# Optimization experiments

Measured on AMD Instinct MI355X. Metric: run time of the kernel, lower is better.

## Reference

```python
import jax, jax.numpy as jnp
import numpy as np

B, T, D, H = 4, 1024, 1024, 16
DH = D // H  # 64

def setup_inputs() -> dict:
    key = jax.random.key(0)
    ks = jax.random.split(key, 5)
    s = 1.0 / np.sqrt(D)
    return {
        "x": jax.random.normal(ks[0], (B, T, D), dtype=jnp.float32),
        "Wqkv": jax.random.uniform(ks[1], (D, 3 * D), dtype=jnp.float32, minval=-s, maxval=s),
        "bqkv": jax.random.uniform(ks[2], (3 * D,), dtype=jnp.float32, minval=-s, maxval=s),
        "Wproj": jax.random.uniform(ks[3], (D, D), dtype=jnp.float32, minval=-s, maxval=s),
        "bproj": jax.random.uniform(ks[4], (D,), dtype=jnp.float32, minval=-s, maxval=s),
        "mask": jnp.ones((B, T), dtype=jnp.int32),
    }

def reference(x, Wqkv, bqkv, Wproj, bproj, mask):
    Bx, Tx, C = x.shape
    qkv = x @ Wqkv + bqkv                      # [B,T,3D]
    q, k, v = jnp.split(qkv, 3, axis=-1)
    # [B,H,T,DH]
    q = q.reshape(Bx, Tx, H, DH).transpose(0, 2, 1, 3)
    k = k.reshape(Bx, Tx, H, DH).transpose(0, 2, 1, 3)
    v = v.reshape(Bx, Tx, H, DH).transpose(0, 2, 1, 3)
    att = jnp.einsum("bhqd,bhkd->bhqk", q, k) / np.sqrt(DH)
    causal = jnp.tril(jnp.ones((Tx, Tx), dtype=bool))          # [T,T]
    keep = causal[None, None] & (mask[:, None, None, :] != 0)  # [B,1,T,T] broadcast
    att = jnp.where(keep, att, -jnp.inf)
    att = jax.nn.softmax(att, axis=-1)
    # dropout is identity in eval / p=0
    out = jnp.einsum("bhqk,bhkd->bhqd", att, v)                # [B,H,T,DH]
    out = out.transpose(0, 2, 1, 3).reshape(Bx, Tx, C)
    return out @ Wproj + bproj
```

## Files before the change

kernel.cpp:

```cpp
#include <hip/hip_runtime.h>
#include <hip/hip_bf16.h>
#include <cstddef>
#include <cstdint>

#define Bb 4
#define Tt 1024
#define Dd 1024
#define Hh 16

typedef __bf16 bf16x8 __attribute__((ext_vector_type(8)));
typedef __bf16 bf16x4 __attribute__((ext_vector_type(4)));
typedef float  f32x4  __attribute__((ext_vector_type(4)));

__device__ __forceinline__ void gload16(const void* g, void* l) {
    __builtin_amdgcn_global_load_lds(
        (const __attribute__((address_space(1))) void*)g,
        (__attribute__((address_space(3))) void*)l, 16, 0, 0);
}

__global__ __launch_bounds__(256) void prep(const float* __restrict__ x,
                                            const float* __restrict__ Wqkv,
                                            const float* __restrict__ Wproj,
                                            __bf16* __restrict__ xb,
                                            __bf16* __restrict__ wqT,
                                            __bf16* __restrict__ wpT) {
    const int bid = blockIdx.x;
    if (bid < 4096) {
        int i = bid * 256 + threadIdx.x;
        float4 v = ((const float4*)x)[i];
        bf16x4 o = { (__bf16)v.x, (__bf16)v.y, (__bf16)v.z, (__bf16)v.w };
        ((bf16x4*)xb)[i] = o;
        return;
    }
    __shared__ float ld[64][65];
    const float* in;
    __bf16* out;
    int K, N, k0, n0;
    if (bid < 4096 + 768) {
        int j = bid - 4096;
        in = Wqkv; out = wqT; K = 1024; N = 3072;
        k0 = (j & 15) * 64; n0 = (j >> 4) * 64;
    } else {
        int j = bid - 4096 - 768;
        in = Wproj; out = wpT; K = 1024; N = 1024;
        k0 = (j & 15) * 64; n0 = (j >> 4) * 64;
    }
    #pragma unroll
    for (int i = 0; i < 16; i++) {
        int idx = i * 256 + threadIdx.x;
        int r = idx >> 6, c = idx & 63;
        ld[r][c] = in[(size_t)(k0 + r) * N + n0 + c];
    }
    __syncthreads();
    #pragma unroll
    for (int i = 0; i < 16; i++) {
        int idx = i * 256 + threadIdx.x;
        int r = idx >> 6, c = idx & 63;
        out[(size_t)(n0 + r) * K + k0 + c] = (__bf16)ld[c][r];
    }
}

__global__ __launch_bounds__(256) void v_transpose(const __bf16* __restrict__ qkv,
                                                   __bf16* __restrict__ vt) {
    __shared__ __bf16 ld[64][65];
    const int t0 = blockIdx.x * 64;
    const int h  = blockIdx.y;
    const int b  = blockIdx.z;
    const size_t src = ((size_t)(b * Tt + t0)) * 3072 + 2048 + h * 64;
    #pragma unroll
    for (int i = 0; i < 16; i++) {
        int idx = i * 256 + threadIdx.x;
        int tr = idx >> 6, dc = idx & 63;
        ld[tr][dc] = qkv[src + (size_t)tr * 3072 + dc];
    }
    __syncthreads();
    const size_t dst = ((size_t)((b * Hh + h) * 64)) * Tt + t0;
    #pragma unroll
    for (int i = 0; i < 16; i++) {
        int idx = i * 256 + threadIdx.x;
        int dr = idx >> 6, tc = idx & 63;
        vt[dst + (size_t)dr * Tt + tc] = ld[tc][dr];
    }
}

__global__ __launch_bounds__(256) void gemm_bf16(const __bf16* __restrict__ A,
                                                 const __bf16* __restrict__ Bt,
                                                 const float* __restrict__ bias,
                                                 void* __restrict__ Cout,
                                                 int M, int N, int K, int mode) {
    __shared__ __align__(16) __bf16 As[128 * 64];
    __shared__ __align__(16) __bf16 Bs[128 * 64];
    const int tid  = threadIdx.x;
    const int lane = tid & 63;
    const int wave = tid >> 6;
    const int wy = wave >> 1, wx = wave & 1;
    const int l15 = lane & 15, quad = lane >> 4;
    const size_t row0 = (size_t)blockIdx.y * 128;
    const size_t col0 = (size_t)blockIdx.x * 128;

    f32x4 acc[4][4] = {};

    for (int k0 = 0; k0 < K; k0 += 64) {
        #pragma unroll
        for (int i = 0; i < 4; i++) {
            int c = i * 256 + tid;
            int r = c >> 3, seg = (c & 7) ^ (r & 7);
            gload16(&A[(row0 + r) * K + k0 + seg * 8], &As[c * 8]);
        }
        #pragma unroll
        for (int i = 0; i < 4; i++) {
            int c = i * 256 + tid;
            int r = c >> 3, seg = (c & 7) ^ (r & 7);
            gload16(&Bt[(col0 + r) * K + k0 + seg * 8], &Bs[c * 8]);
        }
        __syncthreads();
        #pragma unroll
        for (int kc = 0; kc < 2; kc++) {
            bf16x8 af[4], bfr[4];
            #pragma unroll
            for (int i = 0; i < 4; i++)
                af[i] = *(const bf16x8*)&As[(wy * 64 + i * 16 + l15) * 64 +
                                            (((kc * 4 + quad) ^ (l15 & 7)) * 8)];
            #pragma unroll
            for (int j = 0; j < 4; j++)
                bfr[j] = *(const bf16x8*)&Bs[(wx * 64 + j * 16 + l15) * 64 +
                                             (((kc * 4 + quad) ^ (l15 & 7)) * 8)];
            #pragma unroll
            for (int i = 0; i < 4; i++)
                #pragma unroll
                for (int j = 0; j < 4; j++)
                    acc[i][j] = __builtin_amdgcn_mfma_f32_16x16x32_bf16(af[i], bfr[j], acc[i][j], 0, 0, 0);
        }
        __syncthreads();
    }

    #pragma unroll
    for (int j = 0; j < 4; j++) {
        const size_t col = col0 + wx * 64 + j * 16 + l15;
        const float bj = bias[col];
        const float scale = (mode == 1 && col < 1024) ? 0.125f : 1.0f;
        #pragma unroll
        for (int i = 0; i < 4; i++) {
            const size_t row = row0 + wy * 64 + i * 16 + quad * 4;
            #pragma unroll
            for (int r = 0; r < 4; r++) {
                float v = (acc[i][j][r] + bj) * scale;
                if (mode == 1) ((__bf16*)Cout)[(row + r) * N + col] = (__bf16)v;
                else           ((float*)Cout)[(row + r) * N + col] = v;
            }
        }
    }
}

__global__ __launch_bounds__(256) void gemm_bf16_n64(const __bf16* __restrict__ A,
                                                     const __bf16* __restrict__ Bt,
                                                     const float* __restrict__ bias,
                                                     float* __restrict__ Cout,
                                                     int M, int N, int K) {
    __shared__ __align__(16) __bf16 As[128 * 64];
    __shared__ __align__(16) __bf16 Bs[64 * 64];
    const int tid  = threadIdx.x;
    const int lane = tid & 63;
    const int wave = tid >> 6;
    const int wy = wave >> 1, wx = wave & 1;
    const int l15 = lane & 15, quad = lane >> 4;
    const size_t row0 = (size_t)blockIdx.y * 128;
    const size_t col0 = (size_t)blockIdx.x * 64;

    f32x4 acc[4][2] = {};

    for (int k0 = 0; k0 < K; k0 += 64) {
        #pragma unroll
        for (int i = 0; i < 4; i++) {
            int c = i * 256 + tid;
            int r = c >> 3, seg = (c & 7) ^ (r & 7);
            gload16(&A[(row0 + r) * K + k0 + seg * 8], &As[c * 8]);
        }
        #pragma unroll
        for (int i = 0; i < 2; i++) {
            int c = i * 256 + tid;
            int r = c >> 3, seg = (c & 7) ^ (r & 7);
            gload16(&Bt[(col0 + r) * K + k0 + seg * 8], &Bs[c * 8]);
        }
        __syncthreads();
        #pragma unroll
        for (int kc = 0; kc < 2; kc++) {
            bf16x8 af[4], bfr[2];
            #pragma unroll
            for (int i = 0; i < 4; i++)
                af[i] = *(const bf16x8*)&As[(wy * 64 + i * 16 + l15) * 64 +
                                            (((kc * 4 + quad) ^ (l15 & 7)) * 8)];
            #pragma unroll
            for (int j = 0; j < 2; j++)
                bfr[j] = *(const bf16x8*)&Bs[(wx * 32 + j * 16 + l15) * 64 +
                                             (((kc * 4 + quad) ^ (l15 & 7)) * 8)];
            #pragma unroll
            for (int i = 0; i < 4; i++)
                #pragma unroll
                for (int j = 0; j < 2; j++)
                    acc[i][j] = __builtin_amdgcn_mfma_f32_16x16x32_bf16(af[i], bfr[j], acc[i][j], 0, 0, 0);
        }
        __syncthreads();
    }

    #pragma unroll
    for (int j = 0; j < 2; j++) {
        const size_t col = col0 + wx * 32 + j * 16 + l15;
        const float bj = bias[col];
        #pragma unroll
        for (int i = 0; i < 4; i++) {
            const size_t row = row0 + wy * 64 + i * 16 + quad * 4;
            #pragma unroll
            for (int r = 0; r < 4; r++)
                Cout[(row + r) * N + col] = acc[i][j][r] + bj;
        }
    }
}

__global__ __launch_bounds__(256, 4) void attn_mfma(const __bf16* __restrict__ qkv,
                                                    const __bf16* __restrict__ vt,
                                                    const int* __restrict__ mask,
                                                    __bf16* __restrict__ att) {
    __shared__ __align__(16) __bf16 Ks[2][4096];
    __shared__ __align__(16) __bf16 Vs[2][4096];
    __shared__ __align__(16) __bf16 Ps[4][1024];

    const int h  = blockIdx.x & 15;
    const int b  = blockIdx.x >> 4;
    const int qt = 15 - blockIdx.y;
    const int tid = threadIdx.x, lane = tid & 63, wave = tid >> 6;
    const int l15 = lane & 15, quad = lane >> 4;

    #pragma unroll
    for (int i = 0; i < 2; i++) {
        int c = i * 256 + tid;
        int rr = c >> 3, ch = c & 7;
        gload16(&qkv[((size_t)(b * Tt + qt * 64 + rr)) * 3072 + h * 64 + ((ch ^ (rr & 7)) * 8)],
                &Ks[0][c * 8]);
    }
    __syncthreads();
    bf16x8 qf0 = *(const bf16x8*)&Ks[0][(wave * 16 + l15) * 64 + ((quad ^ (l15 & 7)) * 8)];
    bf16x8 qf1 = *(const bf16x8*)&Ks[0][(wave * 16 + l15) * 64 + (((4 + quad) ^ (l15 & 7)) * 8)];
    __syncthreads();

    #pragma unroll
    for (int i = 0; i < 2; i++) {
        int c = i * 256 + tid;
        int rr = c >> 3, ch = c & 7, sw = ((ch ^ (rr & 7)) * 8);
        gload16(&qkv[((size_t)(b * Tt + rr)) * 3072 + 1024 + h * 64 + sw], &Ks[0][c * 8]);
        gload16(&vt[((size_t)((b * Hh + h) * 64 + rr)) * Tt + sw], &Vs[0][c * 8]);
    }

    f32x4 Oacc[4] = {};
    float lsum = 0.0f;

    for (int kt = 0; kt <= qt; kt++) {
        __syncthreads();
        const int cur = kt & 1;
        if (kt < qt) {
            #pragma unroll
            for (int i = 0; i < 2; i++) {
                int c = i * 256 + tid;
                int rr = c >> 3, ch = c & 7, sw = ((ch ^ (rr & 7)) * 8);
                gload16(&qkv[((size_t)(b * Tt + (kt + 1) * 64 + rr)) * 3072 + 1024 + h * 64 + sw],
                        &Ks[cur ^ 1][c * 8]);
                gload16(&vt[((size_t)((b * Hh + h) * 64 + rr)) * Tt + (kt + 1) * 64 + sw],
                        &Vs[cur ^ 1][c * 8]);
            }
        }

        int mv4[4][4];
        #pragma unroll
        for (int j = 0; j < 4; j++) {
            const int4 m4 = *(const int4*)&mask[b * Tt + kt * 64 + j * 16 + quad * 4];
            mv4[j][0] = m4.x; mv4[j][1] = m4.y; mv4[j][2] = m4.z; mv4[j][3] = m4.w;
        }

        bf16x8 ak[4][2];
        #pragma unroll
        for (int j = 0; j < 4; j++)
            #pragma unroll
            for (int kc = 0; kc < 2; kc++)
                ak[j][kc] = *(const bf16x8*)&Ks[cur][(j * 16 + l15) * 64 +
                                                     (((kc * 4 + quad) ^ (l15 & 7)) * 8)];
        #pragma unroll
        for (int j = 0; j < 4; j++) {
            f32x4 st = {};
            st = __builtin_amdgcn_mfma_f32_16x16x32_bf16(ak[j][0], qf0, st, 0, 0, 0);
            st = __builtin_amdgcn_mfma_f32_16x16x32_bf16(ak[j][1], qf1, st, 0, 0, 0);
            bf16x4 pv;
            #pragma unroll
            for (int r = 0; r < 4; r++) {
                const int tloc = j * 16 + quad * 4 + r;
                bool keep = (mv4[j][r] != 0);
                if (kt == qt) keep = keep && (tloc <= wave * 16 + l15);
                const float pe = keep ? __expf(st[r]) : 0.0f;
                lsum += pe;
                pv[r] = (__bf16)pe;
            }
            *(bf16x4*)&Ps[wave][l15 * 64 + (((j * 4 + quad) ^ ((l15 & 7) << 1)) * 4)] = pv;
        }

        bf16x8 av[4][2];
        #pragma unroll
        for (int n = 0; n < 4; n++)
            #pragma unroll
            for (int kc = 0; kc < 2; kc++)
                av[n][kc] = *(const bf16x8*)&Vs[cur][(n * 16 + l15) * 64 +
                                                     (((kc * 4 + quad) ^ (l15 & 7)) * 8)];
        bf16x8 p0 = *(const bf16x8*)&Ps[wave][l15 * 64 + (((2 * quad) ^ ((l15 & 7) << 1)) * 4)];
        bf16x8 p1 = *(const bf16x8*)&Ps[wave][l15 * 64 + (((2 * (4 + quad)) ^ ((l15 & 7) << 1)) * 4)];
        #pragma unroll
        for (int n = 0; n < 4; n++) {
            Oacc[n] = __builtin_amdgcn_mfma_f32_16x16x32_bf16(av[n][0], p0, Oacc[n], 0, 0, 0);
            Oacc[n] = __builtin_amdgcn_mfma_f32_16x16x32_bf16(av[n][1], p1, Oacc[n], 0, 0, 0);
        }
    }

    float lt = lsum;
    lt += __shfl_xor(lt, 16);
    lt += __shfl_xor(lt, 32);
    const float inv = 1.0f / lt;
    const int q = qt * 64 + wave * 16 + l15;
    #pragma unroll
    for (int n = 0; n < 4; n++) {
        bf16x4 o;
        #pragma unroll
        for (int r = 0; r < 4; r++) o[r] = (__bf16)(Oacc[n][r] * inv);
        *(bf16x4*)&att[((size_t)(b * Tt + q)) * Dd + h * 64 + n * 16 + quad * 4] = o;
    }
}

extern "C" void kernel_launch(void* const* d_in, const int* in_sizes, int n_in,
                              void* d_out, int out_size, void* d_ws, size_t ws_size,
                              hipStream_t stream) {
    const float* x     = (const float*)d_in[0];
    const float* Wqkv  = (const float*)d_in[1];
    const float* bqkv  = (const float*)d_in[2];
    const float* Wproj = (const float*)d_in[3];
    const float* bproj = (const float*)d_in[4];
    const int*   mask  = (const int*)d_in[5];
    float* out = (float*)d_out;

    __bf16* xb  = (__bf16*)d_ws;
    __bf16* wqT = xb  + (size_t)4096 * 1024;
    __bf16* wpT = wqT + (size_t)3072 * 1024;
    __bf16* qkv = wpT + (size_t)1024 * 1024;
    __bf16* vt  = qkv + (size_t)4096 * 3072;
    __bf16* att = vt  + (size_t)4 * 16 * 64 * 1024;

    prep<<<4096 + 768 + 256, 256, 0, stream>>>(x, Wqkv, Wproj, xb, wqT, wpT);

    gemm_bf16<<<dim3(24, 32), 256, 0, stream>>>(xb, wqT, bqkv, qkv, 4096, 3072, 1024, 1);

    v_transpose<<<dim3(16, 16, 4), 256, 0, stream>>>(qkv, vt);
    attn_mfma<<<dim3(64, 16), 256, 0, stream>>>(qkv, vt, mask, att);

    gemm_bf16_n64<<<dim3(16, 32), 256, 0, stream>>>(att, wpT, bproj, out, 4096, 1024, 1024);
}
```

Before: 168.7 us.

## Double-buffer GEMM K-loop and stage epilogue through LDS for coalesced stores

Both bf16 GEMMs move from a single-buffered K=64 loop with two barriers per step to a double-buffered K=32 loop. The next tile's global-to-LDS load is issued before the current tile's MFMAs, and each step needs only one barrier. The epilogue now writes bias-added results into padded LDS, then stores them to global memory as 16-byte row-contiguous vectors instead of scattered scalar stores. The mode argument is dropped and the QKV GEMM is hardwired to bf16 output with Q scaling. A smaller K tile means more loop iterations, and the padded LDS rows (132 bf16 / 66 float stride) are only 8-byte aligned on odd rows while being read as 16-byte vectors.

After: 166.4 us. About the same (-1.4%).

```diff
diff --git a/kernel.cpp b/kernel.cpp
--- a/kernel.cpp
+++ b/kernel.cpp
@@ -86,10 +86,12 @@
 __global__ __launch_bounds__(256) void gemm_bf16(const __bf16* __restrict__ A,
                                                  const __bf16* __restrict__ Bt,
                                                  const float* __restrict__ bias,
-                                                 void* __restrict__ Cout,
-                                                 int M, int N, int K, int mode) {
-    __shared__ __align__(16) __bf16 As[128 * 64];
-    __shared__ __align__(16) __bf16 Bs[128 * 64];
+                                                 __bf16* __restrict__ Cout,
+                                                 int M, int N, int K) {
+    __shared__ __align__(16) __bf16 smem[17408];
+    __bf16* const As = smem;
+    __bf16* const Bs = smem + 8192;
+
     const int tid  = threadIdx.x;
     const int lane = tid & 63;
     const int wave = tid >> 6;
@@ -100,55 +102,68 @@
 
     f32x4 acc[4][4] = {};
 
-    for (int k0 = 0; k0 < K; k0 += 64) {
+    #pragma unroll
+    for (int i = 0; i < 2; i++) {
+        int c = i * 256 + tid;
+        int r = c >> 2, seg = (c & 3) ^ ((r >> 1) & 3);
+        gload16(&A[(row0 + r) * K + seg * 8], &As[c * 8]);
+        gload16(&Bt[(col0 + r) * K + seg * 8], &Bs[c * 8]);
+    }
+
+    const int niter = K >> 5;
+    for (int it = 0; it < niter; it++) {
+        __syncthreads();
+        const int cur = it & 1;
+        if (it + 1 < niter) {
+            const int k0 = (it + 1) << 5;
+            #pragma unroll
+            for (int i = 0; i < 2; i++) {
+                int c = i * 256 + tid;
+                int r = c >> 2, seg = (c & 3) ^ ((r >> 1) & 3);
+                gload16(&A[(row0 + r) * K + k0 + seg * 8], &As[(cur ^ 1) * 4096 + c * 8]);
+                gload16(&Bt[(col0 + r) * K + k0 + seg * 8], &Bs[(cur ^ 1) * 4096 + c * 8]);
+            }
+        }
+        bf16x8 af[4], bfr[4];
         #pragma unroll
         for (int i = 0; i < 4; i++) {
-            int c = i * 256 + tid;
-            int r = c >> 3, seg = (c & 7) ^ (r & 7);
-            gload16(&A[(row0 + r) * K + k0 + seg * 8], &As[c * 8]);
-        }
+            const int r = wy * 64 + i * 16 + l15;
+            af[i] = *(const bf16x8*)&As[cur * 4096 + r * 32 + ((quad ^ ((r >> 1) & 3)) * 8)];
+        }
+        #pragma unroll
+        for (int j = 0; j < 4; j++) {
+            const int r = wx * 64 + j * 16 + l15;
+            bfr[j] = *(const bf16x8*)&Bs[cur * 4096 + r * 32 + ((quad ^ ((r >> 1) & 3)) * 8)];
+        }
+        #pragma unroll
+        for (int i = 0; i < 4; i++)
+            #pragma unroll
+            for (int j = 0; j < 4; j++)
+                acc[i][j] = __builtin_amdgcn_mfma_f32_16x16x32_bf16(af[i], bfr[j], acc[i][j], 0, 0, 0);
+    }
+
+    __syncthreads();
+    #pragma unroll
+    for (int j = 0; j < 4; j++) {
+        const int cl = wx * 64 + j * 16 + l15;
+        const size_t col = col0 + cl;
+        const float bj = bias[col];
+        const float scale = (col < 1024) ? 0.125f : 1.0f;
         #pragma unroll
         for (int i = 0; i < 4; i++) {
-            int c = i * 256 + tid;
-            int r = c >> 3, seg = (c & 7) ^ (r & 7);
-            gload16(&Bt[(col0 + r) * K + k0 + seg * 8], &Bs[c * 8]);
-        }
-        __syncthreads();
-        #pragma unroll
-        for (int kc = 0; kc < 2; kc++) {
-            bf16x8 af[4], bfr[4];
-            #pragma unroll
-            for (int i = 0; i < 4; i++)
-                af[i] = *(const bf16x8*)&As[(wy * 64 + i * 16 + l15) * 64 +
-                                            (((kc * 4 + quad) ^ (l15 & 7)) * 8)];
-            #pragma unroll
-            for (int j = 0; j < 4; j++)
-                bfr[j] = *(const bf16x8*)&Bs[(wx * 64 + j * 16 + l15) * 64 +
-                                             (((kc * 4 + quad) ^ (l15 & 7)) * 8)];
-            #pragma unroll
-            for (int i = 0; i < 4; i++)
-                #pragma unroll
-                for (int j = 0; j < 4; j++)
-                    acc[i][j] = __builtin_amdgcn_mfma_f32_16x16x32_bf16(af[i], bfr[j], acc[i][j], 0, 0, 0);
-        }
-        __syncthreads();
-    }
-
-    #pragma unroll
-    for (int j = 0; j < 4; j++) {
-        const size_t col = col0 + wx * 64 + j * 16 + l15;
-        const float bj = bias[col];
-        const float scale = (mode == 1 && col < 1024) ? 0.125f : 1.0f;
-        #pragma unroll
-        for (int i = 0; i < 4; i++) {
-            const size_t row = row0 + wy * 64 + i * 16 + quad * 4;
-            #pragma unroll
-            for (int r = 0; r < 4; r++) {
-                float v = (acc[i][j][r] + bj) * scale;
-                if (mode == 1) ((__bf16*)Cout)[(row + r) * N + col] = (__bf16)v;
-                else           ((float*)Cout)[(row + r) * N + col] = v;
-            }
-        }
+            const int rl = wy * 64 + i * 16 + quad * 4;
+            #pragma unroll
+            for (int r = 0; r < 4; r++)
+                smem[(rl + r) * 132 + cl] = (__bf16)((acc[i][j][r] + bj) * scale);
+        }
+    }
+    __syncthreads();
+    #pragma unroll
+    for (int p = 0; p < 8; p++) {
+        const int row = p * 16 + (tid >> 4);
+        const int ch  = tid & 15;
+        bf16x8 v = *(const bf16x8*)&smem[row * 132 + ch * 8];
+        *(bf16x8*)&Cout[(row0 + row) * N + col0 + ch * 8] = v;
     }
 }
 
@@ -157,8 +172,11 @@
                                                      const float* __restrict__ bias,
                                                      float* __restrict__ Cout,
                                                      int M, int N, int K) {
-    __shared__ __align__(16) __bf16 As[128 * 64];
-    __shared__ __align__(16) __bf16 Bs[64 * 64];
+    __shared__ __align__(16) __bf16 smem[17408];
+    __bf16* const As = smem;
+    __bf16* const Bs = smem + 8192;
+    float* const Ct = (float*)smem;
+
     const int tid  = threadIdx.x;
     const int lane = tid & 63;
     const int wave = tid >> 6;
@@ -169,51 +187,74 @@
 
     f32x4 acc[4][2] = {};
 
-    for (int k0 = 0; k0 < K; k0 += 64) {
+    #pragma unroll
+    for (int i = 0; i < 2; i++) {
+        int c = i * 256 + tid;
+        int r = c >> 2, seg = (c & 3) ^ ((r >> 1) & 3);
+        gload16(&A[(row0 + r) * K + seg * 8], &As[c * 8]);
+    }
+    {
+        int c = tid;
+        int r = c >> 2, seg = (c & 3) ^ ((r >> 1) & 3);
+        gload16(&Bt[(col0 + r) * K + seg * 8], &Bs[c * 8]);
+    }
+
+    const int niter = K >> 5;
+    for (int it = 0; it < niter; it++) {
+        __syncthreads();
+        const int cur = it & 1;
+        if (it + 1 < niter) {
+            const int k0 = (it + 1) << 5;
+            #pragma unroll
+            for (int i = 0; i < 2; i++) {
+                int c = i * 256 + tid;
+                int r = c >> 2, seg = (c & 3) ^ ((r >> 1) & 3);
+                gload16(&A[(row0 + r) * K + k0 + seg * 8], &As[(cur ^ 1) * 4096 + c * 8]);
+            }
+            {
+                int c = tid;
+                int r = c >> 2, seg = (c & 3) ^ ((r >> 1) & 3);
+                gload16(&Bt[(col0 + r) * K + k0 + seg * 8], &Bs[(cur ^ 1) * 2048 + c * 8]);
+            }
+        }
+        bf16x8 af[4], bfr[2];
         #pragma unroll
         for (int i = 0; i < 4; i++) {
-            int c = i * 256 + tid;
-            int r = c >> 3, seg = (c & 7) ^ (r & 7);
-            gload16(&A[(row0 + r) * K + k0 + seg * 8], &As[c * 8]);
-        }
-        #pragma unroll
-        for (int i = 0; i < 2; i++) {
-            int c = i * 256 + tid;
-            int r = c >> 3, seg = (c & 7) ^ (r & 7);
-            gload16(&Bt[(col0 + r) * K + k0 + seg * 8], &Bs[c * 8]);
-        }
-        __syncthreads();
-        #pragma unroll
-        for (int kc = 0; kc < 2; kc++) {
-            bf16x8 af[4], bfr[2];
-            #pragma unroll
-            for (int i = 0; i < 4; i++)
-                af[i] = *(const bf16x8*)&As[(wy * 64 + i * 16 + l15) * 64 +
-                                            (((kc * 4 + quad) ^ (l15 & 7)) * 8)];
+            const int r = wy * 64 + i * 16 + l15;
+            af[i] = *(const bf16x8*)&As[cur * 4096 + r * 32 + ((quad ^ ((r >> 1) & 3)) * 8)];
+        }
+        #pragma unroll
+        for (int j = 0; j < 2; j++) {
+            const int r = wx * 32 + j * 16 + l15;
+            bfr[j] = *(const bf16x8*)&Bs[cur * 2048 + r * 32 + ((quad ^ ((r >> 1) & 3)) * 8)];
+        }
+        #pragma unroll
+        for (int i = 0; i < 4; i++)
             #pragma unroll
             for (int j = 0; j < 2; j++)
-                bfr[j] = *(const bf16x8*)&Bs[(wx * 32 + j * 16 + l15) * 64 +
-                                             (((kc * 4 + quad) ^ (l15 & 7)) * 8)];
-            #pragma unroll
-            for (int i = 0; i < 4; i++)
-                #pragma unroll
-                for (int j = 0; j < 2; j++)
-                    acc[i][j] = __builtin_amdgcn_mfma_f32_16x16x32_bf16(af[i], bfr[j], acc[i][j], 0, 0, 0);
-        }
-        __syncthreads();
-    }
-
+                acc[i][j] = __builtin_amdgcn_mfma_f32_16x16x32_bf16(af[i], bfr[j], acc[i][j], 0, 0, 0);
+    }
+
+    __syncthreads();
     #pragma unroll
     for (int j = 0; j < 2; j++) {
-        const size_t col = col0 + wx * 32 + j * 16 + l15;
-        const float bj = bias[col];
+        const int cl = wx * 32 + j * 16 + l15;
+        const float bj = bias[col0 + cl];
         #pragma unroll
         for (int i = 0; i < 4; i++) {
-            const size_t row = row0 + wy * 64 + i * 16 + quad * 4;
+            const int rl = wy * 64 + i * 16 + quad * 4;
             #pragma unroll
             for (int r = 0; r < 4; r++)
-                Cout[(row + r) * N + col] = acc[i][j][r] + bj;
-        }
+                Ct[(rl + r) * 66 + cl] = acc[i][j][r] + bj;
+        }
+    }
+    __syncthreads();
+    #pragma unroll
+    for (int p = 0; p < 8; p++) {
+        const int row = p * 16 + (tid >> 4);
+        const int ch  = tid & 15;
+        f32x4 v = *(const f32x4*)&Ct[row * 66 + ch * 4];
+        *(f32x4*)&Cout[(row0 + row) * N + col0 + ch * 4] = v;
     }
 }
 
@@ -351,7 +392,7 @@
 
     prep<<<4096 + 768 + 256, 256, 0, stream>>>(x, Wqkv, Wproj, xb, wqT, wpT);
 
-    gemm_bf16<<<dim3(24, 32), 256, 0, stream>>>(xb, wqT, bqkv, qkv, 4096, 3072, 1024, 1);
+    gemm_bf16<<<dim3(24, 32), 256, 0, stream>>>(xb, wqT, bqkv, qkv, 4096, 3072, 1024);
 
     v_transpose<<<dim3(16, 16, 4), 256, 0, stream>>>(qkv, vt);
     attn_mfma<<<dim3(64, 16), 256, 0, stream>>>(qkv, vt, mask, att);
```

## Fuse V transpose into double-buffered QKV GEMM; precompute mask bits via ballot

Applied to the files above, without the earlier changes.

The QKV GEMM now double-buffers a K=32 slice in LDS and stages its output tile through shared memory. This gives coalesced 16-byte stores, and blocks covering the V columns also write the transposed V tensor directly, so the separate v_transpose kernel and its extra pass over memory are removed. The attention kernel builds a per-lane mask bitmap with wave ballots once, then reads it with readlane instead of loading the int mask on every key tile. Shared memory use and epilogue work per GEMM block go up.

After: 163.5 us (median of 2 runs). 1.03x faster.

```diff
diff --git a/kernel.cpp b/kernel.cpp
--- a/kernel.cpp
+++ b/kernel.cpp
@@ -60,36 +60,16 @@
     }
 }
 
-__global__ __launch_bounds__(256) void v_transpose(const __bf16* __restrict__ qkv,
-                                                   __bf16* __restrict__ vt) {
-    __shared__ __bf16 ld[64][65];
-    const int t0 = blockIdx.x * 64;
-    const int h  = blockIdx.y;
-    const int b  = blockIdx.z;
-    const size_t src = ((size_t)(b * Tt + t0)) * 3072 + 2048 + h * 64;
-    #pragma unroll
-    for (int i = 0; i < 16; i++) {
-        int idx = i * 256 + threadIdx.x;
-        int tr = idx >> 6, dc = idx & 63;
-        ld[tr][dc] = qkv[src + (size_t)tr * 3072 + dc];
-    }
-    __syncthreads();
-    const size_t dst = ((size_t)((b * Hh + h) * 64)) * Tt + t0;
-    #pragma unroll
-    for (int i = 0; i < 16; i++) {
-        int idx = i * 256 + threadIdx.x;
-        int dr = idx >> 6, tc = idx & 63;
-        vt[dst + (size_t)dr * Tt + tc] = ld[tc][dr];
-    }
-}
-
-__global__ __launch_bounds__(256) void gemm_bf16(const __bf16* __restrict__ A,
-                                                 const __bf16* __restrict__ Bt,
-                                                 const float* __restrict__ bias,
-                                                 void* __restrict__ Cout,
-                                                 int M, int N, int K, int mode) {
-    __shared__ __align__(16) __bf16 As[128 * 64];
-    __shared__ __align__(16) __bf16 Bs[128 * 64];
+__global__ __launch_bounds__(256) void gemm_qkv(const __bf16* __restrict__ A,
+                                                const __bf16* __restrict__ Bt,
+                                                const float* __restrict__ bias,
+                                                __bf16* __restrict__ Cout,
+                                                __bf16* __restrict__ vt,
+                                                int M, int N, int K) {
+    __shared__ __align__(16) __bf16 smem[17408];
+    __bf16* const As = smem;
+    __bf16* const Bs = smem + 8192;
+
     const int tid  = threadIdx.x;
     const int lane = tid & 63;
     const int wave = tid >> 6;
@@ -100,54 +80,83 @@
 
     f32x4 acc[4][4] = {};
 
-    for (int k0 = 0; k0 < K; k0 += 64) {
+    #pragma unroll
+    for (int i = 0; i < 2; i++) {
+        int c = i * 256 + tid;
+        int r = c >> 2, seg = (c & 3) ^ ((r >> 1) & 3);
+        gload16(&A[(row0 + r) * K + seg * 8], &As[c * 8]);
+        gload16(&Bt[(col0 + r) * K + seg * 8], &Bs[c * 8]);
+    }
+
+    const int niter = K >> 5;
+    for (int it = 0; it < niter; it++) {
+        __syncthreads();
+        const int cur = it & 1;
+        if (it + 1 < niter) {
+            const int k0 = (it + 1) << 5;
+            #pragma unroll
+            for (int i = 0; i < 2; i++) {
+                int c = i * 256 + tid;
+                int r = c >> 2, seg = (c & 3) ^ ((r >> 1) & 3);
+                gload16(&A[(row0 + r) * K + k0 + seg * 8], &As[(cur ^ 1) * 4096 + c * 8]);
+                gload16(&Bt[(col0 + r) * K + k0 + seg * 8], &Bs[(cur ^ 1) * 4096 + c * 8]);
+            }
+        }
+        bf16x8 af[4], bfr[4];
         #pragma unroll
         for (int i = 0; i < 4; i++) {
-            int c = i * 256 + tid;
-            int r = c >> 3, seg = (c & 7) ^ (r & 7);
-            gload16(&A[(row0 + r) * K + k0 + seg * 8], &As[c * 8]);
-        }
+            const int r = wy * 64 + i * 16 + l15;
+            af[i] = *(const bf16x8*)&As[cur * 4096 + r * 32 + ((quad ^ ((r >> 1) & 3)) * 8)];
+        }
+        #pragma unroll
+        for (int j = 0; j < 4; j++) {
+            const int r = wx * 64 + j * 16 + l15;
+            bfr[j] = *(const bf16x8*)&Bs[cur * 4096 + r * 32 + ((quad ^ ((r >> 1) & 3)) * 8)];
+        }
+        #pragma unroll
+        for (int i = 0; i < 4; i++)
+            #pragma unroll
+            for (int j = 0; j < 4; j++)
+                acc[i][j] = __builtin_amdgcn_mfma_f32_16x16x32_bf16(af[i], bfr[j], acc[i][j], 0, 0, 0);
+    }
+
+    __syncthreads();
+    #pragma unroll
+    for (int j = 0; j < 4; j++) {
+        const int cl = wx * 64 + j * 16 + l15;
+        const size_t col = col0 + cl;
+        const float bj = bias[col];
+        const float scale = (col < 1024) ? 0.125f : 1.0f;
         #pragma unroll
         for (int i = 0; i < 4; i++) {
-            int c = i * 256 + tid;
-            int r = c >> 3, seg = (c & 7) ^ (r & 7);
-            gload16(&Bt[(col0 + r) * K + k0 + seg * 8], &Bs[c * 8]);
-        }
-        __syncthreads();
-        #pragma unroll
-        for (int kc = 0; kc < 2; kc++) {
-            bf16x8 af[4], bfr[4];
-            #pragma unroll
-            for (int i = 0; i < 4; i++)
-                af[i] = *(const bf16x8*)&As[(wy * 64 + i * 16 + l15) * 64 +
-                                            (((kc * 4 + quad) ^ (l15 & 7)) * 8)];
-            #pragma unroll
-            for (int j = 0; j < 4; j++)
-                bfr[j] = *(const bf16x8*)&Bs[(wx * 64 + j * 16 + l15) * 64 +
-                                             (((kc * 4 + quad) ^ (l15 & 7)) * 8)];
-            #pragma unroll
-            for (int i = 0; i < 4; i++)
-                #pragma unroll
-                for (int j = 0; j < 4; j++)
-                    acc[i][j] = __builtin_amdgcn_mfma_f32_16x16x32_bf16(af[i], bfr[j], acc[i][j], 0, 0, 0);
-        }
-        __syncthreads();
-    }
-
-    #pragma unroll
-    for (int j = 0; j < 4; j++) {
-        const size_t col = col0 + wx * 64 + j * 16 + l15;
-        const float bj = bias[col];
-        const float scale = (mode == 1 && col < 1024) ? 0.125f : 1.0f;
-        #pragma unroll
-        for (int i = 0; i < 4; i++) {
-            const size_t row = row0 + wy * 64 + i * 16 + quad * 4;
-            #pragma unroll
-            for (int r = 0; r < 4; r++) {
-                float v = (acc[i][j][r] + bj) * scale;
-                if (mode == 1) ((__bf16*)Cout)[(row + r) * N + col] = (__bf16)v;
-                else           ((float*)Cout)[(row + r) * N + col] = v;
-            }
+            const int rl = wy * 64 + i * 16 + quad * 4;
+            #pragma unroll
+            for (int r = 0; r < 4; r++)
+                smem[(rl + r) * 132 + cl] = (__bf16)((acc[i][j][r] + bj) * scale);
+        }
+    }
+    __syncthreads();
+    #pragma unroll
+    for (int p = 0; p < 8; p++) {
+        const int row = p * 16 + (tid >> 4);
+        const int ch  = tid & 15;
+        bf16x8 v = *(const bf16x8*)&smem[row * 132 + ch * 8];
+        *(bf16x8*)&Cout[(row0 + row) * N + col0 + ch * 8] = v;
+    }
+    if (col0 >= 2048) {
+        const int bidx = (int)(row0 >> 10);
+        const int t0g  = (int)(row0 & 1023);
+        const int cl   = tid >> 1;
+        const int half = tid & 1;
+        const int hd   = (int)(col0 - 2048) + cl;
+        const size_t vrow = ((size_t)((bidx * Hh + (hd >> 6)) * 64 + (hd & 63))) * Tt + t0g;
+        #pragma unroll
+        for (int s = 0; s < 8; s++) {
+            const int t = half * 64 + s * 8;
+            bf16x8 v;
+            #pragma unroll
+            for (int u = 0; u < 8; u++) v[u] = smem[(t + u) * 132 + cl];
+            *(bf16x8*)&vt[vrow + t] = v;
         }
     }
 }
@@ -238,6 +247,13 @@
         gload16(&qkv[((size_t)(b * Tt + qt * 64 + rr)) * 3072 + h * 64 + ((ch ^ (rr & 7)) * 8)],
                 &Ks[0][c * 8]);
     }
+
+    uint32_t mlo = 0, mhi = 0;
+    for (int p = 0; p < 16; p++) {
+        unsigned long long bal = __ballot(mask[b * Tt + p * 64 + lane] != 0);
+        if ((lane & 15) == p) { mlo = (uint32_t)bal; mhi = (uint32_t)(bal >> 32); }
+    }
+
     __syncthreads();
     bf16x8 qf0 = *(const bf16x8*)&Ks[0][(wave * 16 + l15) * 64 + ((quad ^ (l15 & 7)) * 8)];
     bf16x8 qf1 = *(const bf16x8*)&Ks[0][(wave * 16 + l15) * 64 + (((4 + quad) ^ (l15 & 7)) * 8)];
@@ -269,12 +285,8 @@
             }
         }
 
-        int mv4[4][4];
-        #pragma unroll
-        for (int j = 0; j < 4; j++) {
-            const int4 m4 = *(const int4*)&mask[b * Tt + kt * 64 + j * 16 + quad * 4];
-            mv4[j][0] = m4.x; mv4[j][1] = m4.y; mv4[j][2] = m4.z; mv4[j][3] = m4.w;
-        }
+        const uint32_t lo = (uint32_t)__builtin_amdgcn_readlane((int)mlo, kt);
+        const uint32_t hi = (uint32_t)__builtin_amdgcn_readlane((int)mhi, kt);
 
         bf16x8 ak[4][2];
         #pragma unroll
@@ -288,11 +300,12 @@
             f32x4 st = {};
             st = __builtin_amdgcn_mfma_f32_16x16x32_bf16(ak[j][0], qf0, st, 0, 0, 0);
             st = __builtin_amdgcn_mfma_f32_16x16x32_bf16(ak[j][1], qf1, st, 0, 0, 0);
+            const uint32_t fld = (j < 2) ? (lo >> (j * 16)) : (hi >> ((j - 2) * 16));
             bf16x4 pv;
             #pragma unroll
             for (int r = 0; r < 4; r++) {
                 const int tloc = j * 16 + quad * 4 + r;
-                bool keep = (mv4[j][r] != 0);
+                bool keep = (fld >> (quad * 4 + r)) & 1;
                 if (kt == qt) keep = keep && (tloc <= wave * 16 + l15);
                 const float pe = keep ? __expf(st[r]) : 0.0f;
                 lsum += pe;
@@ -351,9 +364,8 @@
 
     prep<<<4096 + 768 + 256, 256, 0, stream>>>(x, Wqkv, Wproj, xb, wqT, wpT);
 
-    gemm_bf16<<<dim3(24, 32), 256, 0, stream>>>(xb, wqT, bqkv, qkv, 4096, 3072, 1024, 1);
-
-    v_transpose<<<dim3(16, 16, 4), 256, 0, stream>>>(qkv, vt);
+    gemm_qkv<<<dim3(24, 32), 256, 0, stream>>>(xb, wqT, bqkv, qkv, vt, 4096, 3072, 1024);
+
     attn_mfma<<<dim3(64, 16), 256, 0, stream>>>(qkv, vt, mask, att);
 
     gemm_bf16_n64<<<dim3(16, 32), 256, 0, stream>>>(att, wpT, bproj, out, 4096, 1024, 1024);
```
